# Performance work log

Hardware: AMD Instinct MI355X
Metric: run time of the kernel (lower is better)

## Reference

```python
import jax, jax.numpy as jnp
import numpy as np

K = 9
SIGMA = 4.0
RADIUS = 16  # round(4*sigma)
IMAGE_SHAPE = (256, 256)


def _gaussian_kernel_1d():
    i = jnp.arange(2 * RADIUS + 1, dtype=jnp.float32) - RADIUS
    g = jnp.exp(-(i ** 2) / (2.0 * SIGMA ** 2))
    return g / jnp.sum(g)


def _gaussian_blur(x):
    # x: [b, H, W, 1]; separable Gaussian blur, reflect-101 borders (cv2 default)
    g = _gaussian_kernel_1d()
    xp = jnp.pad(x, ((0, 0), (RADIUS, RADIUS), (RADIUS, RADIUS), (0, 0)), mode='reflect')
    dn = ('NHWC', 'HWIO', 'NHWC')
    kv = g.reshape(2 * RADIUS + 1, 1, 1, 1)  # vertical pass
    kh = g.reshape(1, 2 * RADIUS + 1, 1, 1)  # horizontal pass
    y = jax.lax.conv_general_dilated(xp, kv, (1, 1), 'VALID', dimension_numbers=dn)
    y = jax.lax.conv_general_dilated(y, kh, (1, 1), 'VALID', dimension_numbers=dn)
    return y


def setup_inputs() -> dict:
    key = jax.random.key(0)
    k1, k2 = jax.random.split(key)
    inputs = jax.random.normal(k1, (8, 32, 32, 512), dtype=jnp.float32)
    feature_vector = jax.random.normal(k2, (16384, 512), dtype=jnp.float32)
    return {"inputs": inputs, "feature_vector": feature_vector}


def reference(inputs, feature_vector):
    b, h, w, c = inputs.shape
    feat = inputs.reshape(b * h * w, c)
    # pairwise euclidean distances: [b*h*w, N]
    d2 = (jnp.sum(feat ** 2, axis=-1, keepdims=True)
          + jnp.sum(feature_vector ** 2, axis=-1)[None, :]
          - 2.0 * feat @ feature_vector.T)
    dist = jnp.sqrt(jnp.maximum(d2, 0.0))
    # k smallest distances, ascending (equivalent to tf.sort(...)[..., :k])
    neg_topk, _ = jax.lax.top_k(-dist, K)
    score = -neg_topk  # [b*h*w, K], ascending
    mask = score[:, 0].reshape(b, h, w, 1)
    score = score.reshape(b, h * w, K)
    # patch with maximal nearest-neighbor distance
    idx = jnp.argmax(score[..., 0], axis=-1)  # [b]
    conf = jnp.take_along_axis(score, idx[:, None, None], axis=1)[:, 0, :]  # [b, K]
    exp_conf = jnp.exp(conf)
    weight = 1.0 - jnp.max(exp_conf, axis=-1) / jnp.sum(exp_conf, axis=-1)
    score_out = (jnp.max(score[..., 0], axis=-1) * weight)[:, None]  # [b, 1]
    mask = jax.image.resize(mask, (b, *IMAGE_SHAPE, 1), method='bilinear', antialias=False)
    mask = _gaussian_blur(mask)
    return score_out, mask
```

## Files before the change

### kernel.cpp

```cpp
#include <hip/hip_runtime.h>

typedef __attribute__((ext_vector_type(8))) short bf16x8;
typedef __attribute__((ext_vector_type(4))) float f32x4;

static constexpr int M = 8192;
static constexpr int N = 16384;
static constexpr int K = 512;
static constexpr int BM = 128;
static constexpr int BN = 128;
static constexpr int BK = 32;
static constexpr int KSTEPS = K / BK;
static constexpr int RBLK = M / BM;
static constexpr int CBLK = N / BN;
static constexpr int BMs = 128;
static constexpr int BKs = 64;
static constexpr int KCHUNKS_S = K / BKs;
static constexpr int NGROUPS_S = 8;
static constexpr int GROUP_N_S = N / NGROUPS_S;
static constexpr int NTILES_S = GROUP_N_S / 128;
static constexpr float F_INF = 3.0e38f;

__device__ __forceinline__ unsigned short f2bf(float f) {
    unsigned int u = __float_as_uint(f);
    return (unsigned short)((u + 0x7fffu + ((u >> 16) & 1u)) >> 16);
}

__device__ __forceinline__ void gl_lds16(const unsigned short* g, unsigned short* l) {
    __builtin_amdgcn_global_load_lds(
        (const __attribute__((address_space(1))) unsigned int*)g,
        (__attribute__((address_space(3))) unsigned int*)l, 16, 0, 0);
}

__global__ void k_prep(const float* __restrict__ Q, const float* __restrict__ F,
                       unsigned short* __restrict__ Qb, unsigned short* __restrict__ Fb,
                       float* __restrict__ qn, float* __restrict__ fn) {
    int wid = blockIdx.x * 4 + (threadIdx.x >> 6);
    int lane = threadIdx.x & 63;
    bool isQ = wid < M;
    const float* src = isQ ? (Q + (size_t)wid * K) : (F + (size_t)(wid - M) * K);
    unsigned short* dst = isQ ? (Qb + (size_t)wid * K) : (Fb + (size_t)(wid - M) * K);
    const float4* p = reinterpret_cast<const float4*>(src) + lane * 2;
    float4 a = p[0], b = p[1];
    float s = a.x*a.x + a.y*a.y + a.z*a.z + a.w*a.w
            + b.x*b.x + b.y*b.y + b.z*b.z + b.w*b.w;
    bf16x8 v;
    v[0]=(short)f2bf(a.x); v[1]=(short)f2bf(a.y); v[2]=(short)f2bf(a.z); v[3]=(short)f2bf(a.w);
    v[4]=(short)f2bf(b.x); v[5]=(short)f2bf(b.y); v[6]=(short)f2bf(b.z); v[7]=(short)f2bf(b.w);
    *reinterpret_cast<bf16x8*>(dst + lane * 8) = v;
    #pragma unroll
    for (int d = 1; d < 64; d <<= 1) s += __shfl_xor(s, d);
    if (lane == 0) { if (isQ) qn[wid] = s; else fn[wid - M] = s; }
}

__global__ void k_norms(const float* __restrict__ Q, const float* __restrict__ F,
                        float* __restrict__ qn, float* __restrict__ fn) {
    int wid = blockIdx.x * 4 + (threadIdx.x >> 6);
    int lane = threadIdx.x & 63;
    const float* src = (wid < M) ? (Q + (size_t)wid * K) : (F + (size_t)(wid - M) * K);
    const float4* p = reinterpret_cast<const float4*>(src) + lane * 2;
    float4 a = p[0], b = p[1];
    float s = a.x*a.x + a.y*a.y + a.z*a.z + a.w*a.w
            + b.x*b.x + b.y*b.y + b.z*b.z + b.w*b.w;
    #pragma unroll
    for (int d = 1; d < 64; d <<= 1) s += __shfl_xor(s, d);
    if (lane == 0) { if (wid < M) qn[wid] = s; else fn[wid - M] = s; }
}

__global__ __launch_bounds__(256, 4)
void k_mingemm4(const unsigned short* __restrict__ Qb, const unsigned short* __restrict__ Fb,
                const float* __restrict__ qn, const float* __restrict__ fn,
                float* __restrict__ pv, unsigned int* __restrict__ pi) {
    __shared__ unsigned short As[2][BM * BK];
    __shared__ unsigned short Bs[2][BN * BK];
    __shared__ float redv[BM][2];
    __shared__ unsigned int redi[BM][2];

    const int tid = threadIdx.x;
    const int lane = tid & 63;
    const int wave = tid >> 6;
    const int wr = wave >> 1, wc = wave & 1;
    const int l15 = lane & 15, l4 = lane >> 4;

    const int wg = blockIdx.x;
    const int x = wg & 7, q = wg >> 3;
    const int c_blk = x * 16 + (q & 15);
    const int r_blk = q >> 4;
    const int row0 = r_blk * BM;
    const int col0 = c_blk * BN;

    const int row_l = lane >> 2, p4 = lane & 3;
    const int g4 = p4 ^ (row_l & 3);
    const unsigned short* gA[2];
    const unsigned short* gB[2];
    #pragma unroll
    for (int i = 0; i < 2; ++i) {
        int row = wave * 32 + i * 16 + row_l;
        gA[i] = Qb + (size_t)(row0 + row) * K + g4 * 8;
        gB[i] = Fb + (size_t)(col0 + row) * K + g4 * 8;
    }

    auto stage = [&](int kc, int buf) {
        #pragma unroll
        for (int i = 0; i < 2; ++i) gl_lds16(gA[i] + kc * BK, &As[buf][(wave*32 + i*16) * BK]);
        #pragma unroll
        for (int i = 0; i < 2; ++i) gl_lds16(gB[i] + kc * BK, &Bs[buf][(wave*32 + i*16) * BK]);
    };

    f32x4 acc[4][4];
    #pragma unroll
    for (int a = 0; a < 4; ++a)
        #pragma unroll
        for (int b = 0; b < 4; ++b) acc[a][b] = f32x4{0.f, 0.f, 0.f, 0.f};

    stage(0, 0);
    __syncthreads();

    int cur = 0;
    for (int kc = 0; kc < KSTEPS; ++kc) {
        if (kc + 1 < KSTEPS) stage(kc + 1, cur ^ 1);
        __builtin_amdgcn_sched_barrier(0);
        const int gidx = l4;
        bf16x8 af[4], bfv[4];
        #pragma unroll
        for (int fi = 0; fi < 4; ++fi) {
            int r = wr*64 + fi*16 + l15;
            int pg = gidx ^ (r & 3);
            af[fi] = *reinterpret_cast<const bf16x8*>(&As[cur][r*BK + pg*8]);
        }
        #pragma unroll
        for (int fj = 0; fj < 4; ++fj) {
            int r = wc*64 + fj*16 + l15;
            int pg = gidx ^ (r & 3);
            bfv[fj] = *reinterpret_cast<const bf16x8*>(&Bs[cur][r*BK + pg*8]);
        }
        __builtin_amdgcn_s_setprio(1);
        #pragma unroll
        for (int fi = 0; fi < 4; ++fi)
            #pragma unroll
            for (int fj = 0; fj < 4; ++fj)
                acc[fi][fj] = __builtin_amdgcn_mfma_f32_16x16x32_bf16(
                    af[fi], bfv[fj], acc[fi][fj], 0, 0, 0);
        __builtin_amdgcn_s_setprio(0);
        __syncthreads();
        cur ^= 1;
    }

    float fnv[4];
    #pragma unroll
    for (int fj = 0; fj < 4; ++fj) fnv[fj] = fn[col0 + wc*64 + fj*16 + l15];
    #pragma unroll
    for (int fi = 0; fi < 4; ++fi) {
        #pragma unroll
        for (int j = 0; j < 4; ++j) {
            int rloc = wr*64 + fi*16 + l4*4 + j;
            float qv = qn[row0 + rloc];
            float v = F_INF; unsigned int ix = 0;
            #pragma unroll
            for (int fj = 0; fj < 4; ++fj) {
                float d2 = qv + fnv[fj] - 2.0f * acc[fi][fj][j];
                if (d2 < v) { v = d2; ix = (unsigned int)(col0 + wc*64 + fj*16 + l15); }
            }
            #pragma unroll
            for (int d = 1; d < 16; d <<= 1) {
                float ov = __shfl_xor(v, d);
                unsigned int oi = (unsigned int)__shfl_xor((int)ix, d);
                if (ov < v) { v = ov; ix = oi; }
            }
            if (l15 == 0) { redv[rloc][wc] = v; redi[rloc][wc] = ix; }
        }
    }
    __syncthreads();
    if (tid < BM) {
        float v = redv[tid][0]; unsigned int ix = redi[tid][0];
        if (redv[tid][1] < v) { v = redv[tid][1]; ix = redi[tid][1]; }
        pv[(size_t)(row0 + tid) * CBLK + c_blk] = v;
        pi[(size_t)(row0 + tid) * CBLK + c_blk] = ix;
    }
}

__global__ __launch_bounds__(256, 2)
void k_mingemm_cast(const float* __restrict__ Q, const float* __restrict__ F,
                    const float* __restrict__ qn, const float* __restrict__ fn,
                    float* __restrict__ pv, unsigned int* __restrict__ pi) {
    __shared__ unsigned short As[BMs * BKs];
    __shared__ unsigned short Bs[BMs * BKs];
    __shared__ float qn_t[BMs];
    __shared__ float fn_t[BMs];

    const int tid = threadIdx.x;
    const int lane = tid & 63;
    const int wave = tid >> 6;
    const int wr = wave >> 1, wc = wave & 1;
    const int l15 = lane & 15, l4 = lane >> 4;

    const int row0 = blockIdx.x * BMs;
    const int gbase = blockIdx.y * GROUP_N_S;

    const int srow = tid >> 3;
    const int p8 = tid & 7;
    const int g8 = p8 ^ (srow & 7);
    const float* pA[4];
    const float* pB[4];
    int dstOff[4];
    #pragma unroll
    for (int i = 0; i < 4; ++i) {
        int r = i * 32 + srow;
        pA[i] = Q + (size_t)(row0 + r) * K + g8 * 8;
        pB[i] = F + (size_t)(gbase + r) * K + g8 * 8;
        dstOff[i] = r * BKs + p8 * 8;
    }

    float mval[4][4];
    unsigned int midx[4][4];
    float qnv[4][4];
    #pragma unroll
    for (int a = 0; a < 4; ++a)
        #pragma unroll
        for (int b = 0; b < 4; ++b) { mval[a][b] = F_INF; midx[a][b] = 0; qnv[a][b] = 0.f; }

    for (int nt = 0; nt < NTILES_S; ++nt) {
        f32x4 acc[4][4];
        #pragma unroll
        for (int a = 0; a < 4; ++a)
            #pragma unroll
            for (int b = 0; b < 4; ++b) acc[a][b] = f32x4{0.f, 0.f, 0.f, 0.f};

        for (int kc = 0; kc < KCHUNKS_S; ++kc) {
            __syncthreads();
            #pragma unroll
            for (int i = 0; i < 4; ++i) {
                const float4* sa = reinterpret_cast<const float4*>(pA[i] + kc * BKs);
                float4 xa = sa[0], ya = sa[1];
                const float4* sb = reinterpret_cast<const float4*>(pB[i] + nt * (128 * K) + kc * BKs);
                float4 xb = sb[0], yb = sb[1];
                bf16x8 va, vb;
                va[0]=(short)f2bf(xa.x); va[1]=(short)f2bf(xa.y); va[2]=(short)f2bf(xa.z); va[3]=(short)f2bf(xa.w);
                va[4]=(short)f2bf(ya.x); va[5]=(short)f2bf(ya.y); va[6]=(short)f2bf(ya.z); va[7]=(short)f2bf(ya.w);
                vb[0]=(short)f2bf(xb.x); vb[1]=(short)f2bf(xb.y); vb[2]=(short)f2bf(xb.z); vb[3]=(short)f2bf(xb.w);
                vb[4]=(short)f2bf(yb.x); vb[5]=(short)f2bf(yb.y); vb[6]=(short)f2bf(yb.z); vb[7]=(short)f2bf(yb.w);
                *reinterpret_cast<bf16x8*>(&As[dstOff[i]]) = va;
                *reinterpret_cast<bf16x8*>(&Bs[dstOff[i]]) = vb;
            }
            if (kc == 0) {
                if (nt == 0 && tid < BMs) qn_t[tid] = qn[row0 + tid];
                if (tid < 128) fn_t[tid] = fn[gbase + nt * 128 + tid];
            }
            __syncthreads();
            if (nt == 0 && kc == 0) {
                #pragma unroll
                for (int fi = 0; fi < 4; ++fi)
                    #pragma unroll
                    for (int j = 0; j < 4; ++j)
                        qnv[fi][j] = qn_t[wr*64 + fi*16 + l4*4 + j];
            }
            #pragma unroll
            for (int ks = 0; ks < 2; ++ks) {
                const int gidx = ks * 4 + l4;
                bf16x8 af[4], bfv[4];
                #pragma unroll
                for (int fi = 0; fi < 4; ++fi) {
                    int r = wr*64 + fi*16 + l15;
                    int pg = gidx ^ (r & 7);
                    af[fi] = *reinterpret_cast<const bf16x8*>(&As[r*BKs + pg*8]);
                }
                #pragma unroll
                for (int fj = 0; fj < 4; ++fj) {
                    int r = wc*64 + fj*16 + l15;
                    int pg = gidx ^ (r & 7);
                    bfv[fj] = *reinterpret_cast<const bf16x8*>(&Bs[r*BKs + pg*8]);
                }
                #pragma unroll
                for (int fi = 0; fi < 4; ++fi)
                    #pragma unroll
                    for (int fj = 0; fj < 4; ++fj)
                        acc[fi][fj] = __builtin_amdgcn_mfma_f32_16x16x32_bf16(
                            af[fi], bfv[fj], acc[fi][fj], 0, 0, 0);
            }
        }
        const int colb = gbase + nt * 128 + wc * 64;
        float fnv[4];
        #pragma unroll
        for (int fj = 0; fj < 4; ++fj) fnv[fj] = fn_t[wc*64 + fj*16 + l15];
        #pragma unroll
        for (int fi = 0; fi < 4; ++fi) {
            #pragma unroll
            for (int j = 0; j < 4; ++j) {
                float qv = qnv[fi][j];
                #pragma unroll
                for (int fj = 0; fj < 4; ++fj) {
                    float d2 = qv + fnv[fj] - 2.0f * acc[fi][fj][j];
                    if (d2 < mval[fi][j]) {
                        mval[fi][j] = d2;
                        midx[fi][j] = (unsigned int)(colb + fj*16 + l15);
                    }
                }
            }
        }
    }
    #pragma unroll
    for (int fi = 0; fi < 4; ++fi) {
        #pragma unroll
        for (int j = 0; j < 4; ++j) {
            float v = mval[fi][j];
            unsigned int ix = midx[fi][j];
            #pragma unroll
            for (int d = 1; d < 16; d <<= 1) {
                float ov = __shfl_xor(v, d);
                unsigned int oi = (unsigned int)__shfl_xor((int)ix, d);
                if (ov < v) { v = ov; ix = oi; }
            }
            if (l15 == 0) {
                int rg = row0 + wr*64 + fi*16 + l4*4 + j;
                int pidx = rg * 16 + blockIdx.y * 2 + wc;
                pv[pidx] = v;
                pi[pidx] = ix;
            }
        }
    }
}

__global__ void k_refine(const float* __restrict__ Q, const float* __restrict__ F,
                         const float* __restrict__ pv, const unsigned int* __restrict__ pi,
                         float* __restrict__ minD, int PS) {
    int row = blockIdx.x * 4 + (threadIdx.x >> 6);
    int lane = threadIdx.x & 63;
    float v = F_INF; unsigned int ix = 0;
    for (int t = lane; t < PS; t += 64) {
        float nv = pv[(size_t)row*PS + t];
        if (nv < v) { v = nv; ix = pi[(size_t)row*PS + t]; }
    }
    #pragma unroll
    for (int d = 1; d < 64; d <<= 1) {
        float ov = __shfl_xor(v, d);
        unsigned int oi = (unsigned int)__shfl_xor((int)ix, d);
        if (ov < v) { v = ov; ix = oi; }
    }
    const float4* q = reinterpret_cast<const float4*>(Q + (size_t)row * K) + lane*2;
    const float4* f = reinterpret_cast<const float4*>(F + (size_t)ix * K) + lane*2;
    float4 a0 = q[0], a1 = q[1], b0 = f[0], b1 = f[1];
    float s = 0.f, dx;
    dx = a0.x-b0.x; s += dx*dx;  dx = a0.y-b0.y; s += dx*dx;
    dx = a0.z-b0.z; s += dx*dx;  dx = a0.w-b0.w; s += dx*dx;
    dx = a1.x-b1.x; s += dx*dx;  dx = a1.y-b1.y; s += dx*dx;
    dx = a1.z-b1.z; s += dx*dx;  dx = a1.w-b1.w; s += dx*dx;
    #pragma unroll
    for (int d = 1; d < 64; d <<= 1) s += __shfl_xor(s, d);
    if (lane == 0) minD[row] = sqrtf(s);
}

__global__ void k_argmax(const float* __restrict__ minD, unsigned int* __restrict__ sel) {
    __shared__ float sv[256];
    __shared__ int si[256];
    int b = blockIdx.x, tid = threadIdx.x;
    float bv = -F_INF; int bi = 0;
    for (int p = tid; p < 1024; p += 256) {
        float v = minD[b*1024 + p];
        if (v > bv) { bv = v; bi = p; }
    }
    sv[tid] = bv; si[tid] = bi;
    __syncthreads();
    for (int s = 128; s > 0; s >>= 1) {
        if (tid < s) {
            if (sv[tid+s] > sv[tid] || (sv[tid+s] == sv[tid] && si[tid+s] < si[tid])) {
                sv[tid] = sv[tid+s]; si[tid] = si[tid+s];
            }
        }
        __syncthreads();
    }
    if (tid == 0) sel[b] = (unsigned int)(b*1024 + si[0]);
}

__global__ void k_dist8(const float* __restrict__ Q, const float* __restrict__ F,
                        const unsigned int* __restrict__ sel, float* __restrict__ d2all) {
    __shared__ float qs[8][512];
    int tid = threadIdx.x;
    int lane = tid & 63, wave = tid >> 6;
    for (int i = tid; i < 8*512; i += 256) {
        int b = i >> 9;
        qs[b][i & 511] = Q[(size_t)sel[b] * K + (i & 511)];
    }
    __syncthreads();
    int base = blockIdx.x * 128 + wave * 32;
    for (int r = 0; r < 32; ++r) {
        int row = base + r;
        const float4* fp = reinterpret_cast<const float4*>(F + (size_t)row * K) + lane*2;
        float4 f0 = fp[0], f1 = fp[1];
        float fv[8] = {f0.x,f0.y,f0.z,f0.w,f1.x,f1.y,f1.z,f1.w};
        float accb[8];
        #pragma unroll
        for (int b = 0; b < 8; ++b) {
            float s = 0.f;
            #pragma unroll
            for (int e = 0; e < 8; ++e) {
                float d = fv[e] - qs[b][lane*8 + e];
                s += d * d;
            }
            accb[b] = s;
        }
        #pragma unroll
        for (int d = 1; d < 64; d <<= 1)
            #pragma unroll
            for (int b = 0; b < 8; ++b) accb[b] += __shfl_xor(accb[b], d);
        if (lane == 0) {
            #pragma unroll
            for (int b = 0; b < 8; ++b) d2all[b * N + row] = accb[b];
        }
    }
}

__global__ void k_sel9(const float* __restrict__ d2all, float* __restrict__ out) {
    __shared__ float sv[256 * 10];
    int b = blockIdx.x, tid = threadIdx.x;
    float v[9];
    #pragma unroll
    for (int i = 0; i < 9; ++i) v[i] = F_INF;
    for (int i = tid; i < N; i += 256) {
        float x = d2all[b * N + i];
        #pragma unroll
        for (int s = 0; s < 9; ++s) {
            float lo = fminf(v[s], x), hi = fmaxf(v[s], x);
            v[s] = lo; x = hi;
        }
    }
    #pragma unroll
    for (int i = 0; i < 9; ++i) sv[tid*10 + i] = v[i];
    sv[tid*10 + 9] = F_INF;
    __syncthreads();
    for (int s = 128; s > 0; s >>= 1) {
        if (tid < s) {
            int ia = 1, ib = 1;
            float av = sv[tid*10], bv = sv[(tid+s)*10];
            float c[9];
            #pragma unroll
            for (int k = 0; k < 9; ++k) {
                bool ta = av <= bv;
                c[k] = ta ? av : bv;
                float na = sv[tid*10 + ia], nb = sv[(tid+s)*10 + ib];
                if (ta) { av = na; ++ia; } else { bv = nb; ++ib; }
            }
            #pragma unroll
            for (int k = 0; k < 9; ++k) sv[tid*10 + k] = c[k];
        }
        __syncthreads();
    }
    if (tid == 0) {
        float c[9];
        #pragma unroll
        for (int i = 0; i < 9; ++i) c[i] = sqrtf(fmaxf(sv[i], 0.f));
        float S = 0.f;
        #pragma unroll
        for (int i = 0; i < 9; ++i) S += expf(c[i] - c[8]);
        out[b] = c[0] * (1.f - 1.f / S);
    }
}

__global__ void k_top9(const float* __restrict__ Q, const float* __restrict__ F,
                       const unsigned int* __restrict__ sel, float* __restrict__ part9) {
    __shared__ float qs[512];
    __shared__ float dist[2048];
    __shared__ float rv[256];
    __shared__ int ri[256];
    int b = blockIdx.x >> 3, g = blockIdx.x & 7;
    int tid = threadIdx.x;
    unsigned int srow = sel[b];
    if (tid < 128)
        reinterpret_cast<float4*>(qs)[tid] =
            reinterpret_cast<const float4*>(Q + (size_t)srow * K)[tid];
    __syncthreads();
    #pragma unroll
    for (int e = 0; e < 8; ++e) {
        int fl = tid + 256*e;
        const float* fp = F + (size_t)(g*2048 + fl) * K;
        float s = 0.f;
        for (int k = 0; k < 512; k += 4) {
            float4 fv4 = *reinterpret_cast<const float4*>(fp + k);
            float d0 = qs[k]   - fv4.x;
            float d1 = qs[k+1] - fv4.y;
            float d2 = qs[k+2] - fv4.z;
            float d3 = qs[k+3] - fv4.w;
            s += d0*d0 + d1*d1 + d2*d2 + d3*d3;
        }
        dist[fl] = s;
    }
    __syncthreads();
    for (int it = 0; it < 9; ++it) {
        float lv = F_INF; int li = 0;
        #pragma unroll
        for (int e = 0; e < 8; ++e) {
            int idx = tid + 256*e;
            float v = dist[idx];
            if (v < lv) { lv = v; li = idx; }
        }
        rv[tid] = lv; ri[tid] = li;
        __syncthreads();
        for (int s = 128; s > 0; s >>= 1) {
            if (tid < s && rv[tid+s] < rv[tid]) { rv[tid] = rv[tid+s]; ri[tid] = ri[tid+s]; }
            __syncthreads();
        }
        if (tid == 0) {
            part9[(b*8+g)*9 + it] = rv[0];
            dist[ri[0]] = F_INF;
        }
        __syncthreads();
    }
}

__global__ void k_final(const float* __restrict__ part9, float* __restrict__ out) {
    int b = threadIdx.x;
    if (b >= 8) return;
    float arr[9];
    #pragma unroll
    for (int i = 0; i < 9; ++i) arr[i] = F_INF;
    for (int g = 0; g < 8; ++g)
        for (int i = 0; i < 9; ++i) {
            float v = part9[(b*8+g)*9 + i];
            #pragma unroll
            for (int s = 0; s < 9; ++s) {
                float lo = fminf(arr[s], v), hi = fmaxf(arr[s], v);
                arr[s] = lo; v = hi;
            }
        }
    float c[9];
    #pragma unroll
    for (int i = 0; i < 9; ++i) c[i] = sqrtf(fmaxf(arr[i], 0.f));
    float c8 = c[8], S = 0.f;
    #pragma unroll
    for (int i = 0; i < 9; ++i) S += expf(c[i] - c8);
    float w = 1.f - 1.f / S;
    out[b] = c[0] * w;
}

__global__ void k_wmat(float* __restrict__ W) {
    int idx = blockIdx.x * 256 + threadIdx.x;
    int o = idx >> 5, j = idx & 31;
    float gsum = 0.f;
    #pragma unroll
    for (int u = 0; u < 33; ++u) { float d = (float)(u - 16); gsum += expf(-d*d * (1.f/32.f)); }
    float acc = 0.f;
    for (int u = 0; u < 33; ++u) {
        float d = (float)(u - 16);
        float gu = expf(-d*d * (1.f/32.f));
        int y = o + u - 16;
        y = y < 0 ? -y : (y > 255 ? 510 - y : y);
        float xin = ((float)y + 0.5f) * 0.125f - 0.5f;
        float j0f = floorf(xin);
        int j0 = (int)j0f;
        float wfr = xin - j0f;
        float r;
        if (j0 < 0) r = (j == 0) ? 1.f : 0.f;
        else if (j0 >= 31) r = (j == 31) ? 1.f : 0.f;
        else r = (j == j0) ? (1.f - wfr) : ((j == j0 + 1) ? wfr : 0.f);
        acc += gu * r;
    }
    W[idx] = acc / gsum;
}

__global__ void k_mask(const float* __restrict__ minD, const float* __restrict__ W,
                       float* __restrict__ outm) {
    __shared__ float Ms[1024];
    __shared__ float Ws[8192];
    __shared__ float Ts[8192];
    int b = blockIdx.x, tid = threadIdx.x;
    for (int i = tid; i < 1024; i += 256) Ms[i] = minD[b*1024 + i];
    for (int i = tid; i < 8192; i += 256) Ws[i] = W[i];
    __syncthreads();
    {
        int o = tid;
        float wrow[32];
        #pragma unroll
        for (int i = 0; i < 32; ++i) wrow[i] = Ws[o*32 + i];
        for (int j = 0; j < 32; ++j) {
            float s = 0.f;
            #pragma unroll
            for (int i = 0; i < 32; ++i) s += wrow[i] * Ms[i*32 + j];
            Ts[o*32 + j] = s;
        }
    }
    __syncthreads();
    {
        int p = tid;
        float wp[32];
        #pragma unroll
        for (int j = 0; j < 32; ++j) wp[j] = Ws[p*32 + j];
        float* dst = outm + (size_t)b * 65536;
        for (int o = 0; o < 256; ++o) {
            float s = 0.f;
            #pragma unroll
            for (int j = 0; j < 32; ++j) s += Ts[o*32 + j] * wp[j];
            dst[o*256 + p] = s;
        }
    }
}

extern "C" void kernel_launch(void* const* d_in, const int* in_sizes, int n_in,
                              void* d_out, int out_size, void* d_ws, size_t ws_size,
                              hipStream_t stream) {
    const float* Q = (const float*)d_in[0];
    const float* F = (const float*)d_in[1];
    float* out = (float*)d_out;

    const size_t smallFloats = (size_t)8192*CBLK*2 + 8192 + 8 + 576 + (size_t)8*N + 8192 + 16384 + 8192;
    const size_t REQ = smallFloats*4 + (size_t)M*K*2 + (size_t)N*K*2;
    const bool fast = ws_size >= REQ;
    const int PS = fast ? CBLK : 16;

    float* ws = (float*)d_ws;
    float* pv = ws;
    unsigned int* pi = (unsigned int*)(pv + 8192*CBLK);
    float* minD = (float*)(pi + 8192*CBLK);
    unsigned int* sel = (unsigned int*)(minD + 8192);
    float* part9 = (float*)(sel + 8);
    float* d2all = part9 + 576;
    float* qn = d2all + (size_t)8*N;
    float* fn = qn + 8192;
    float* W  = fn + 16384;
    unsigned short* Qb = (unsigned short*)(W + 8192);
    unsigned short* Fb = Qb + (size_t)M*K;

    k_wmat <<<dim3(32), 256, 0, stream>>>(W);
    if (fast) {
        k_prep <<<dim3((M + N) / 4), 256, 0, stream>>>(Q, F, Qb, Fb, qn, fn);
        k_mingemm4<<<dim3(RBLK * CBLK), 256, 0, stream>>>(Qb, Fb, qn, fn, pv, pi);
        k_refine<<<dim3(M / 4), 256, 0, stream>>>(Q, F, pv, pi, minD, PS);
        k_argmax<<<dim3(8), 256, 0, stream>>>(minD, sel);
        k_dist8<<<dim3(N / 128), 256, 0, stream>>>(Q, F, sel, d2all);
        k_sel9 <<<dim3(8), 256, 0, stream>>>(d2all, out);
    } else {
        k_norms<<<dim3((M + N) / 4), 256, 0, stream>>>(Q, F, qn, fn);
        k_mingemm_cast<<<dim3(M / BMs, NGROUPS_S), 256, 0, stream>>>(Q, F, qn, fn, pv, pi);
        k_refine<<<dim3(M / 4), 256, 0, stream>>>(Q, F, pv, pi, minD, PS);
        k_argmax<<<dim3(8), 256, 0, stream>>>(minD, sel);
        k_top9 <<<dim3(64), 256, 0, stream>>>(Q, F, sel, part9);
        k_final<<<dim3(1), 64, 0, stream>>>(part9, out);
    }
    k_mask <<<dim3(8), 256, 0, stream>>>(minD, W, out + 8);
}
```

Baseline: 367.0 us.

## Enlarge min-GEMM tile to 256x256 and stream B fragments from global into registers

The distance GEMM moves to 256x256x64 tiles with 8 waves per block. B (the feature bank) is written by the prep kernel in a fragment-packed layout, so each wave loads its MFMA operands directly from global memory into registers with double buffering, skipping LDS. Only A is staged through LDS, using a wider XOR swizzle and manual vmcnt/barrier pipelining. This raises arithmetic intensity and cuts LDS traffic, at the cost of higher register pressure and a fragile hand-written wait-count schedule.

Measured after the change: 367.0 us. No clear change (-0.0%).

```diff
diff --git a/kernel.cpp b/kernel.cpp
--- a/kernel.cpp
+++ b/kernel.cpp
@@ -6,9 +6,9 @@
 static constexpr int M = 8192;
 static constexpr int N = 16384;
 static constexpr int K = 512;
-static constexpr int BM = 128;
-static constexpr int BN = 128;
-static constexpr int BK = 32;
+static constexpr int BM = 256;
+static constexpr int BN = 256;
+static constexpr int BK = 64;
 static constexpr int KSTEPS = K / BK;
 static constexpr int RBLK = M / BM;
 static constexpr int CBLK = N / BN;
@@ -31,14 +31,20 @@
         (__attribute__((address_space(3))) unsigned int*)l, 16, 0, 0);
 }
 
+__device__ __forceinline__ bf16x8 gload16(const unsigned short* base, unsigned int voff) {
+    bf16x8 r;
+    asm volatile("global_load_dwordx4 %0, %1, %2"
+                 : "=v"(r) : "v"(voff), "s"(base) : "memory");
+    return r;
+}
+
 __global__ void k_prep(const float* __restrict__ Q, const float* __restrict__ F,
-                       unsigned short* __restrict__ Qb, unsigned short* __restrict__ Fb,
+                       unsigned short* __restrict__ Qb, unsigned short* __restrict__ Fbf,
                        float* __restrict__ qn, float* __restrict__ fn) {
     int wid = blockIdx.x * 4 + (threadIdx.x >> 6);
     int lane = threadIdx.x & 63;
     bool isQ = wid < M;
     const float* src = isQ ? (Q + (size_t)wid * K) : (F + (size_t)(wid - M) * K);
-    unsigned short* dst = isQ ? (Qb + (size_t)wid * K) : (Fb + (size_t)(wid - M) * K);
     const float4* p = reinterpret_cast<const float4*>(src) + lane * 2;
     float4 a = p[0], b = p[1];
     float s = a.x*a.x + a.y*a.y + a.z*a.z + a.w*a.w
@@ -46,7 +52,13 @@
     bf16x8 v;
     v[0]=(short)f2bf(a.x); v[1]=(short)f2bf(a.y); v[2]=(short)f2bf(a.z); v[3]=(short)f2bf(a.w);
     v[4]=(short)f2bf(b.x); v[5]=(short)f2bf(b.y); v[6]=(short)f2bf(b.z); v[7]=(short)f2bf(b.w);
-    *reinterpret_cast<bf16x8*>(dst + lane * 8) = v;
+    if (isQ) {
+        *reinterpret_cast<bf16x8*>(Qb + (size_t)wid * K + lane * 8) = v;
+    } else {
+        int f = wid - M;
+        size_t off = ((size_t)(f >> 4) * 16 + (lane >> 2)) * 512 + (f & 15) * 32 + (lane & 3) * 8;
+        *reinterpret_cast<bf16x8*>(Fbf + off) = v;
+    }
     #pragma unroll
     for (int d = 1; d < 64; d <<= 1) s += __shfl_xor(s, d);
     if (lane == 0) { if (isQ) qn[wid] = s; else fn[wid - M] = s; }
@@ -66,93 +78,140 @@
     if (lane == 0) { if (wid < M) qn[wid] = s; else fn[wid - M] = s; }
 }
 
-__global__ __launch_bounds__(256, 4)
-void k_mingemm4(const unsigned short* __restrict__ Qb, const unsigned short* __restrict__ Fb,
+__global__ __launch_bounds__(512, 2)
+void k_mingemm5(const unsigned short* __restrict__ Qb, const unsigned short* __restrict__ Fbf,
                 const float* __restrict__ qn, const float* __restrict__ fn,
                 float* __restrict__ pv, unsigned int* __restrict__ pi) {
     __shared__ unsigned short As[2][BM * BK];
-    __shared__ unsigned short Bs[2][BN * BK];
-    __shared__ float redv[BM][2];
-    __shared__ unsigned int redi[BM][2];
+    __shared__ float redv[BM][4];
+    __shared__ unsigned int redi[BM][4];
 
     const int tid = threadIdx.x;
     const int lane = tid & 63;
     const int wave = tid >> 6;
-    const int wr = wave >> 1, wc = wave & 1;
+    const int wr = wave >> 2;
+    const int wc = wave & 3;
     const int l15 = lane & 15, l4 = lane >> 4;
 
     const int wg = blockIdx.x;
     const int x = wg & 7, q = wg >> 3;
-    const int c_blk = x * 16 + (q & 15);
-    const int r_blk = q >> 4;
+    const int c_blk = x * 8 + (q & 7);
+    const int r_blk = q >> 3;
     const int row0 = r_blk * BM;
     const int col0 = c_blk * BN;
 
-    const int row_l = lane >> 2, p4 = lane & 3;
-    const int g4 = p4 ^ (row_l & 3);
-    const unsigned short* gA[2];
-    const unsigned short* gB[2];
-    #pragma unroll
-    for (int i = 0; i < 2; ++i) {
-        int row = wave * 32 + i * 16 + row_l;
-        gA[i] = Qb + (size_t)(row0 + row) * K + g4 * 8;
-        gB[i] = Fb + (size_t)(col0 + row) * K + g4 * 8;
-    }
-
-    auto stage = [&](int kc, int buf) {
-        #pragma unroll
-        for (int i = 0; i < 2; ++i) gl_lds16(gA[i] + kc * BK, &As[buf][(wave*32 + i*16) * BK]);
-        #pragma unroll
-        for (int i = 0; i < 2; ++i) gl_lds16(gB[i] + kc * BK, &Bs[buf][(wave*32 + i*16) * BK]);
-    };
-
-    f32x4 acc[4][4];
-    #pragma unroll
-    for (int a = 0; a < 4; ++a)
+    const int r_l = lane >> 3, p8 = lane & 7;
+    const int g8 = p8 ^ r_l;
+    const unsigned short* gA[4];
+    #pragma unroll
+    for (int i = 0; i < 4; ++i) {
+        int row = wave * 32 + i * 8 + r_l;
+        gA[i] = Qb + (size_t)(row0 + row) * K + g8 * 8;
+    }
+
+    unsigned int voffB[4][2];
+    #pragma unroll
+    for (int fj = 0; fj < 4; ++fj) {
+        unsigned int nblk = (unsigned int)(c_blk * 16 + wc * 4 + fj);
+        #pragma unroll
+        for (int ks = 0; ks < 2; ++ks)
+            voffB[fj][ks] = (nblk * 16 + ks) * 1024 + l15 * 64 + l4 * 16;
+    }
+
+    f32x4 acc[8][4];
+    #pragma unroll
+    for (int a = 0; a < 8; ++a)
         #pragma unroll
         for (int b = 0; b < 4; ++b) acc[a][b] = f32x4{0.f, 0.f, 0.f, 0.f};
 
-    stage(0, 0);
-    __syncthreads();
-
-    int cur = 0;
-    for (int kc = 0; kc < KSTEPS; ++kc) {
-        if (kc + 1 < KSTEPS) stage(kc + 1, cur ^ 1);
-        __builtin_amdgcn_sched_barrier(0);
-        const int gidx = l4;
-        bf16x8 af[4], bfv[4];
-        #pragma unroll
-        for (int fi = 0; fi < 4; ++fi) {
-            int r = wr*64 + fi*16 + l15;
-            int pg = gidx ^ (r & 3);
-            af[fi] = *reinterpret_cast<const bf16x8*>(&As[cur][r*BK + pg*8]);
-        }
-        #pragma unroll
-        for (int fj = 0; fj < 4; ++fj) {
-            int r = wc*64 + fj*16 + l15;
-            int pg = gidx ^ (r & 3);
-            bfv[fj] = *reinterpret_cast<const bf16x8*>(&Bs[cur][r*BK + pg*8]);
-        }
-        __builtin_amdgcn_s_setprio(1);
-        #pragma unroll
-        for (int fi = 0; fi < 4; ++fi)
-            #pragma unroll
-            for (int fj = 0; fj < 4; ++fj)
-                acc[fi][fj] = __builtin_amdgcn_mfma_f32_16x16x32_bf16(
-                    af[fi], bfv[fj], acc[fi][fj], 0, 0, 0);
-        __builtin_amdgcn_s_setprio(0);
-        __syncthreads();
-        cur ^= 1;
-    }
-
+    bf16x8 b0[4][2], b1[4][2];
+
+    #pragma unroll
+    for (int fj = 0; fj < 4; ++fj) {
+        b0[fj][0] = gload16(Fbf, voffB[fj][0]);
+        b0[fj][1] = gload16(Fbf, voffB[fj][1]);
+    }
+    #pragma unroll
+    for (int i = 0; i < 4; ++i) gl_lds16(gA[i], &As[0][(wave*32 + i*8) * BK]);
+
+#define GSTEP(T, BCUR, BNXT, P) do {                                              \
+    if ((T) < KSTEPS - 1) {                                                       \
+        _Pragma("unroll")                                                         \
+        for (int fj = 0; fj < 4; ++fj) {                                          \
+            BNXT[fj][0] = gload16(Fbf, voffB[fj][0] + ((T)+1)*2048u);             \
+            BNXT[fj][1] = gload16(Fbf, voffB[fj][1] + ((T)+1)*2048u);             \
+        }                                                                         \
+        _Pragma("unroll")                                                         \
+        for (int i = 0; i < 4; ++i)                                               \
+            gl_lds16(gA[i] + ((T)+1)*BK, &As[1-(P)][(wave*32 + i*8) * BK]);       \
+        asm volatile("s_waitcnt vmcnt(12)" ::: "memory");                         \
+    } else {                                                                      \
+        asm volatile("s_waitcnt vmcnt(0)" ::: "memory");                          \
+    }                                                                             \
+    __builtin_amdgcn_sched_barrier(0);                                            \
+    __builtin_amdgcn_s_barrier();                   \
+    __builtin_amdgcn_sched_barrier(0);                                            \
+    {                                                                             \
+        bf16x8 af0[8];                                                            \
+        _Pragma("unroll")                                                         \
+        for (int fi = 0; fi < 8; ++fi) {                                          \
+            int r = wr*128 + fi*16 + l15;                                         \
+            int pg = l4 ^ (r & 7);                                                \
+            af0[fi] = *reinterpret_cast<const bf16x8*>(&As[P][r*BK + pg*8]);      \
+        }                                                                         \
+        asm volatile("s_waitcnt lgkmcnt(0)" ::: "memory");                        \
+        __builtin_amdgcn_sched_barrier(0);                                        \
+        __builtin_amdgcn_s_setprio(1);                                            \
+        _Pragma("unroll")                                                         \
+        for (int fi = 0; fi < 8; ++fi)                                            \
+            _Pragma("unroll")                                                     \
+            for (int fj = 0; fj < 4; ++fj)                                        \
+                acc[fi][fj] = __builtin_amdgcn_mfma_f32_16x16x32_bf16(            \
+                    af0[fi], BCUR[fj][0], acc[fi][fj], 0, 0, 0);                  \
+        __builtin_amdgcn_s_setprio(0);                                            \
+    }                                                                             \
+    {                                                                             \
+        bf16x8 af1[8];                                                            \
+        _Pragma("unroll")                                                         \
+        for (int fi = 0; fi < 8; ++fi) {                                          \
+            int r = wr*128 + fi*16 + l15;                                         \
+            int pg = (4 + l4) ^ (r & 7);                                          \
+            af1[fi] = *reinterpret_cast<const bf16x8*>(&As[P][r*BK + pg*8]);      \
+        }                                                                         \
+        asm volatile("s_waitcnt lgkmcnt(0)" ::: "memory");                        \
+        __builtin_amdgcn_sched_barrier(0);                                        \
+        __builtin_amdgcn_s_barrier();                \
+        __builtin_amdgcn_sched_barrier(0);                                        \
+        __builtin_amdgcn_s_setprio(1);                                            \
+        _Pragma("unroll")                                                         \
+        for (int fi = 0; fi < 8; ++fi)                                            \
+            _Pragma("unroll")                                                     \
+            for (int fj = 0; fj < 4; ++fj)                                        \
+                acc[fi][fj] = __builtin_amdgcn_mfma_f32_16x16x32_bf16(            \
+                    af1[fi], BCUR[fj][1], acc[fi][fj], 0, 0, 0);                  \
+        __builtin_amdgcn_s_setprio(0);                                            \
+    }                                                                             \
+} while (0)
+
+    GSTEP(0, b0, b1, 0);
+    GSTEP(1, b1, b0, 1);
+    GSTEP(2, b0, b1, 0);
+    GSTEP(3, b1, b0, 1);
+    GSTEP(4, b0, b1, 0);
+    GSTEP(5, b1, b0, 1);
+    GSTEP(6, b0, b1, 0);
+    GSTEP(7, b1, b0, 1);
+#undef GSTEP
+
+    __syncthreads();
     float fnv[4];
     #pragma unroll
     for (int fj = 0; fj < 4; ++fj) fnv[fj] = fn[col0 + wc*64 + fj*16 + l15];
     #pragma unroll
-    for (int fi = 0; fi < 4; ++fi) {
+    for (int fi = 0; fi < 8; ++fi) {
         #pragma unroll
         for (int j = 0; j < 4; ++j) {
-            int rloc = wr*64 + fi*16 + l4*4 + j;
+            int rloc = wr*128 + fi*16 + l4*4 + j;
             float qv = qn[row0 + rloc];
             float v = F_INF; unsigned int ix = 0;
             #pragma unroll
@@ -172,7 +231,11 @@
     __syncthreads();
     if (tid < BM) {
         float v = redv[tid][0]; unsigned int ix = redi[tid][0];
-        if (redv[tid][1] < v) { v = redv[tid][1]; ix = redi[tid][1]; }
+        #pragma unroll
+        for (int w2 = 1; w2 < 4; ++w2) {
+            float ov = redv[tid][w2];
+            if (ov < v) { v = ov; ix = redi[tid][w2]; }
+        }
         pv[(size_t)(row0 + tid) * CBLK + c_blk] = v;
         pi[(size_t)(row0 + tid) * CBLK + c_blk] = ix;
     }
@@ -615,12 +678,12 @@
     float* fn = qn + 8192;
     float* W  = fn + 16384;
     unsigned short* Qb = (unsigned short*)(W + 8192);
-    unsigned short* Fb = Qb + (size_t)M*K;
+    unsigned short* Fbf = Qb + (size_t)M*K;
 
     k_wmat <<<dim3(32), 256, 0, stream>>>(W);
     if (fast) {
-        k_prep <<<dim3((M + N) / 4), 256, 0, stream>>>(Q, F, Qb, Fb, qn, fn);
-        k_mingemm4<<<dim3(RBLK * CBLK), 256, 0, stream>>>(Qb, Fb, qn, fn, pv, pi);
+        k_prep <<<dim3((M + N) / 4), 256, 0, stream>>>(Q, F, Qb, Fbf, qn, fn);
+        k_mingemm5<<<dim3(RBLK * CBLK), 512, 0, stream>>>(Qb, Fbf, qn, fn, pv, pi);
         k_refine<<<dim3(M / 4), 256, 0, stream>>>(Q, F, pv, pi, minD, PS);
         k_argmax<<<dim3(8), 256, 0, stream>>>(minD, sel);
         k_dist8<<<dim3(N / 128), 256, 0, stream>>>(Q, F, sel, d2all);
```

## Replace 128x128 min-GEMM with 256x256 8-wave ping-pong pipelined kernel

Applied to the files above, without the earlier changes.

Replaces the 4-wave 128x128-tile bf16 min-distance GEMM with an 8-wave 256x256-tile kernel. It uses BK=64 chunks split into half-tiles and streams them into LDS through a multi-stage global_load_lds schedule. Explicit s_barrier/vmcnt phases interleave MFMA work with prefetch. The larger tiles raise arithmetic intensity and halve the number of per-row partial minima that k_refine must scan, at the cost of more registers, more LDS, one block per CU, and a fragile hand-scheduled pipeline.

Measured after the change: 355.8 us. 3.0% less time.

```diff
diff --git a/kernel.cpp b/kernel.cpp
--- a/kernel.cpp
+++ b/kernel.cpp
@@ -6,10 +6,8 @@
 static constexpr int M = 8192;
 static constexpr int N = 16384;
 static constexpr int K = 512;
-static constexpr int BM = 128;
-static constexpr int BN = 128;
-static constexpr int BK = 32;
-static constexpr int KSTEPS = K / BK;
+static constexpr int BM = 256;
+static constexpr int BN = 256;
 static constexpr int RBLK = M / BM;
 static constexpr int CBLK = N / BN;
 static constexpr int BMs = 128;
@@ -25,7 +23,7 @@
     return (unsigned short)((u + 0x7fffu + ((u >> 16) & 1u)) >> 16);
 }
 
-__device__ __forceinline__ void gl_lds16(const unsigned short* g, unsigned short* l) {
+__device__ __forceinline__ void gl_lds16(const void* g, void* l) {
     __builtin_amdgcn_global_load_lds(
         (const __attribute__((address_space(1))) unsigned int*)g,
         (__attribute__((address_space(3))) unsigned int*)l, 16, 0, 0);
@@ -66,99 +64,152 @@
     if (lane == 0) { if (wid < M) qn[wid] = s; else fn[wid - M] = s; }
 }
 
-__global__ __launch_bounds__(256, 4)
-void k_mingemm4(const unsigned short* __restrict__ Qb, const unsigned short* __restrict__ Fb,
+__global__ __launch_bounds__(512, 1)
+void k_mingemm8(const unsigned short* __restrict__ Qb, const unsigned short* __restrict__ Fb,
                 const float* __restrict__ qn, const float* __restrict__ fn,
                 float* __restrict__ pv, unsigned int* __restrict__ pi) {
-    __shared__ unsigned short As[2][BM * BK];
-    __shared__ unsigned short Bs[2][BN * BK];
-    __shared__ float redv[BM][2];
-    __shared__ unsigned int redi[BM][2];
+    __shared__ unsigned short As[2][2][8192];
+    __shared__ unsigned short Bs[2][2][8192];
+    __shared__ float redv[256][4];
+    __shared__ unsigned int redi[256][4];
 
     const int tid = threadIdx.x;
     const int lane = tid & 63;
     const int wave = tid >> 6;
-    const int wr = wave >> 1, wc = wave & 1;
-    const int l15 = lane & 15, l4 = lane >> 4;
+    const int wr = wave >> 2;
+    const int wc = wave & 3;
+    const int l15 = lane & 15, l4 = lane >> 4, l7 = lane & 7;
+    const int r3 = lane >> 3;
+    const int g8 = (lane & 7) ^ (r3 & 7);
 
     const int wg = blockIdx.x;
     const int x = wg & 7, q = wg >> 3;
-    const int c_blk = x * 16 + (q & 15);
-    const int r_blk = q >> 4;
+    const int c_blk = x * 8 + (q & 7);
+    const int r_blk = q >> 3;
     const int row0 = r_blk * BM;
     const int col0 = c_blk * BN;
 
-    const int row_l = lane >> 2, p4 = lane & 3;
-    const int g4 = p4 ^ (row_l & 3);
-    const unsigned short* gA[2];
-    const unsigned short* gB[2];
-    #pragma unroll
-    for (int i = 0; i < 2; ++i) {
-        int row = wave * 32 + i * 16 + row_l;
-        gA[i] = Qb + (size_t)(row0 + row) * K + g4 * 8;
-        gB[i] = Fb + (size_t)(col0 + row) * K + g4 * 8;
-    }
-
-    auto stage = [&](int kc, int buf) {
-        #pragma unroll
-        for (int i = 0; i < 2; ++i) gl_lds16(gA[i] + kc * BK, &As[buf][(wave*32 + i*16) * BK]);
-        #pragma unroll
-        for (int i = 0; i < 2; ++i) gl_lds16(gB[i] + kc * BK, &Bs[buf][(wave*32 + i*16) * BK]);
-    };
-
-    f32x4 acc[4][4];
-    #pragma unroll
-    for (int a = 0; a < 4; ++a)
+#define STAGE_A(t, hh) do {                                                        \
+    _Pragma("unroll")                                                              \
+    for (int i = 0; i < 2; ++i)                                                    \
+        gl_lds16(Qb + (size_t)(row0 + (hh)*128 + i*64 + wave*8 + r3) * K           \
+                    + (t)*64 + g8*8,                                               \
+                 &As[(t)&1][hh][(i*64 + wave*8) * 64]);                            \
+} while (0)
+#define STAGE_B(t, hh) do {                                                        \
+    _Pragma("unroll")                                                              \
+    for (int i = 0; i < 2; ++i)                                                    \
+        gl_lds16(Fb + (size_t)(col0 + (hh)*128 + i*64 + wave*8 + r3) * K           \
+                    + (t)*64 + g8*8,                                               \
+                 &Bs[(t)&1][hh][(i*64 + wave*8) * 64]);                            \
+} while (0)
+
+    f32x4 acc[8][4];
+    #pragma unroll
+    for (int a = 0; a < 8; ++a)
         #pragma unroll
         for (int b = 0; b < 4; ++b) acc[a][b] = f32x4{0.f, 0.f, 0.f, 0.f};
 
-    stage(0, 0);
-    __syncthreads();
-
-    int cur = 0;
-    for (int kc = 0; kc < KSTEPS; ++kc) {
-        if (kc + 1 < KSTEPS) stage(kc + 1, cur ^ 1);
-        __builtin_amdgcn_sched_barrier(0);
-        const int gidx = l4;
-        bf16x8 af[4], bfv[4];
-        #pragma unroll
-        for (int fi = 0; fi < 4; ++fi) {
-            int r = wr*64 + fi*16 + l15;
-            int pg = gidx ^ (r & 3);
-            af[fi] = *reinterpret_cast<const bf16x8*>(&As[cur][r*BK + pg*8]);
-        }
-        #pragma unroll
-        for (int fj = 0; fj < 4; ++fj) {
-            int r = wc*64 + fj*16 + l15;
-            int pg = gidx ^ (r & 3);
-            bfv[fj] = *reinterpret_cast<const bf16x8*>(&Bs[cur][r*BK + pg*8]);
-        }
-        __builtin_amdgcn_s_setprio(1);
-        #pragma unroll
-        for (int fi = 0; fi < 4; ++fi)
-            #pragma unroll
-            for (int fj = 0; fj < 4; ++fj)
-                acc[fi][fj] = __builtin_amdgcn_mfma_f32_16x16x32_bf16(
-                    af[fi], bfv[fj], acc[fi][fj], 0, 0, 0);
-        __builtin_amdgcn_s_setprio(0);
-        __syncthreads();
-        cur ^= 1;
-    }
+    bf16x8 afr[4][2], bfr[4][2];
+
+#define PHASE(t, s, STMT, VMN) do {                                                \
+    STMT;                                                                          \
+    if ((s) == 0) {                                                                \
+        _Pragma("unroll")                                                          \
+        for (int f = 0; f < 4; ++f)                                                \
+            _Pragma("unroll")                                                      \
+            for (int ks = 0; ks < 2; ++ks)                                         \
+                afr[f][ks] = *reinterpret_cast<const bf16x8*>(                     \
+                    &As[(t)&1][wr][(f*16 + l15)*64 + (((ks*4 + l4) ^ l7))*8]);     \
+        _Pragma("unroll")                                                          \
+        for (int f = 0; f < 4; ++f)                                                \
+            _Pragma("unroll")                                                      \
+            for (int ks = 0; ks < 2; ++ks)                                         \
+                bfr[f][ks] = *reinterpret_cast<const bf16x8*>(                     \
+                    &Bs[(t)&1][f >> 1][(wc*32 + (f & 1)*16 + l15)*64               \
+                                       + (((ks*4 + l4) ^ l7))*8]);                 \
+    } else if ((s) == 2) {                                                         \
+        _Pragma("unroll")                                                          \
+        for (int f = 0; f < 4; ++f)                                                \
+            _Pragma("unroll")                                                      \
+            for (int ks = 0; ks < 2; ++ks)                                         \
+                afr[f][ks] = *reinterpret_cast<const bf16x8*>(                     \
+                    &As[(t)&1][wr][((f+4)*16 + l15)*64 + (((ks*4 + l4) ^ l7))*8]); \
+    }                                                                              \
+    __builtin_amdgcn_s_barrier();                                                  \
+    if ((s) == 0 || (s) == 2) {                                                    \
+        asm volatile("s_waitcnt lgkmcnt(0)" ::: "memory");                         \
+        __builtin_amdgcn_sched_barrier(0);                                         \
+    }                                                                              \
+    __builtin_amdgcn_s_setprio(1);                                                 \
+    {                                                                              \
+        const int AB = ((s) >= 2) ? 4 : 0;                                         \
+        const int FJ = ((s) & 1) ? 2 : 0;                                          \
+        _Pragma("unroll")                                                          \
+        for (int f = 0; f < 4; ++f)                                                \
+            _Pragma("unroll")                                                      \
+            for (int j2 = 0; j2 < 2; ++j2)                                         \
+                _Pragma("unroll")                                                  \
+                for (int ks = 0; ks < 2; ++ks)                                     \
+                    acc[AB + f][FJ + j2] = __builtin_amdgcn_mfma_f32_16x16x32_bf16(\
+                        afr[f][ks], bfr[FJ + j2][ks], acc[AB + f][FJ + j2], 0,0,0);\
+    }                                                                              \
+    __builtin_amdgcn_s_setprio(0);                                                 \
+    asm volatile("s_waitcnt vmcnt(" #VMN ")" ::: "memory");                        \
+    __builtin_amdgcn_sched_barrier(0);                                             \
+    __builtin_amdgcn_s_barrier();                                                  \
+} while (0)
+
+    STAGE_B(0, 0); STAGE_B(0, 1); STAGE_A(0, 0); STAGE_A(0, 1);
+    STAGE_B(1, 0); STAGE_B(1, 1); STAGE_A(1, 0);
+    asm volatile("s_waitcnt vmcnt(6)" ::: "memory");
+    __builtin_amdgcn_sched_barrier(0);
+    __builtin_amdgcn_s_barrier();
+
+#define ITER(T)                                        \
+    PHASE(T,     0, STAGE_A((T)+1, 1), 6);             \
+    PHASE(T,     1, STAGE_B((T)+2, 0), 6);             \
+    PHASE(T,     2, STAGE_B((T)+2, 1), 6);             \
+    PHASE(T,     3, STAGE_A((T)+2, 0), 6);             \
+    PHASE((T)+1, 0, STAGE_A((T)+2, 1), 6);             \
+    PHASE((T)+1, 1, STAGE_B((T)+3, 0), 6);             \
+    PHASE((T)+1, 2, STAGE_B((T)+3, 1), 6);             \
+    PHASE((T)+1, 3, STAGE_A((T)+3, 0), 6);
+
+    ITER(0)
+    ITER(2)
+    ITER(4)
+    PHASE(6, 0, STAGE_A(7, 1), 6);
+    PHASE(6, 1, (void)0, 6);
+    PHASE(6, 2, (void)0, 6);
+    PHASE(6, 3, (void)0, 0);
+    PHASE(7, 0, (void)0, 0);
+    PHASE(7, 1, (void)0, 0);
+    PHASE(7, 2, (void)0, 0);
+    PHASE(7, 3, (void)0, 0);
+#undef ITER
+#undef PHASE
+#undef STAGE_A
+#undef STAGE_B
 
     float fnv[4];
-    #pragma unroll
-    for (int fj = 0; fj < 4; ++fj) fnv[fj] = fn[col0 + wc*64 + fj*16 + l15];
-    #pragma unroll
-    for (int fi = 0; fi < 4; ++fi) {
+    int colg[4];
+    #pragma unroll
+    for (int fj = 0; fj < 4; ++fj) {
+        colg[fj] = col0 + (fj < 2 ? wc*32 + fj*16 : 128 + wc*32 + (fj - 2)*16) + l15;
+        fnv[fj] = fn[colg[fj]];
+    }
+    #pragma unroll
+    for (int fi = 0; fi < 8; ++fi) {
         #pragma unroll
         for (int j = 0; j < 4; ++j) {
-            int rloc = wr*64 + fi*16 + l4*4 + j;
+            int rloc = wr*128 + fi*16 + l4*4 + j;
             float qv = qn[row0 + rloc];
             float v = F_INF; unsigned int ix = 0;
             #pragma unroll
             for (int fj = 0; fj < 4; ++fj) {
                 float d2 = qv + fnv[fj] - 2.0f * acc[fi][fj][j];
-                if (d2 < v) { v = d2; ix = (unsigned int)(col0 + wc*64 + fj*16 + l15); }
+                if (d2 < v) { v = d2; ix = (unsigned int)colg[fj]; }
             }
             #pragma unroll
             for (int d = 1; d < 16; d <<= 1) {
@@ -172,7 +223,11 @@
     __syncthreads();
     if (tid < BM) {
         float v = redv[tid][0]; unsigned int ix = redi[tid][0];
-        if (redv[tid][1] < v) { v = redv[tid][1]; ix = redi[tid][1]; }
+        #pragma unroll
+        for (int w2 = 1; w2 < 4; ++w2) {
+            float ov = redv[tid][w2];
+            if (ov < v) { v = ov; ix = redi[tid][w2]; }
+        }
         pv[(size_t)(row0 + tid) * CBLK + c_blk] = v;
         pi[(size_t)(row0 + tid) * CBLK + c_blk] = ix;
     }
@@ -599,15 +654,14 @@
     const float* F = (const float*)d_in[1];
     float* out = (float*)d_out;
 
-    const size_t smallFloats = (size_t)8192*CBLK*2 + 8192 + 8 + 576 + (size_t)8*N + 8192 + 16384 + 8192;
+    const size_t smallFloats = (size_t)8192*64*2 + 8192 + 8 + 576 + (size_t)8*N + 8192 + 16384 + 8192;
     const size_t REQ = smallFloats*4 + (size_t)M*K*2 + (size_t)N*K*2;
     const bool fast = ws_size >= REQ;
-    const int PS = fast ? CBLK : 16;
 
     float* ws = (float*)d_ws;
     float* pv = ws;
-    unsigned int* pi = (unsigned int*)(pv + 8192*CBLK);
-    float* minD = (float*)(pi + 8192*CBLK);
+    unsigned int* pi = (unsigned int*)(pv + 8192*64);
+    float* minD = (float*)(pi + 8192*64);
     unsigned int* sel = (unsigned int*)(minD + 8192);
     float* part9 = (float*)(sel + 8);
     float* d2all = part9 + 576;
@@ -620,15 +674,15 @@
     k_wmat <<<dim3(32), 256, 0, stream>>>(W);
     if (fast) {
         k_prep <<<dim3((M + N) / 4), 256, 0, stream>>>(Q, F, Qb, Fb, qn, fn);
-        k_mingemm4<<<dim3(RBLK * CBLK), 256, 0, stream>>>(Qb, Fb, qn, fn, pv, pi);
-        k_refine<<<dim3(M / 4), 256, 0, stream>>>(Q, F, pv, pi, minD, PS);
+        k_mingemm8<<<dim3(RBLK * CBLK), 512, 0, stream>>>(Qb, Fb, qn, fn, pv, pi);
+        k_refine<<<dim3(M / 4), 256, 0, stream>>>(Q, F, pv, pi, minD, 64);
         k_argmax<<<dim3(8), 256, 0, stream>>>(minD, sel);
         k_dist8<<<dim3(N / 128), 256, 0, stream>>>(Q, F, sel, d2all);
         k_sel9 <<<dim3(8), 256, 0, stream>>>(d2all, out);
     } else {
         k_norms<<<dim3((M + N) / 4), 256, 0, stream>>>(Q, F, qn, fn);
         k_mingemm_cast<<<dim3(M / BMs, NGROUPS_S), 256, 0, stream>>>(Q, F, qn, fn, pv, pi);
-        k_refine<<<dim3(M / 4), 256, 0, stream>>>(Q, F, pv, pi, minD, PS);
+        k_refine<<<dim3(M / 4), 256, 0, stream>>>(Q, F, pv, pi, minD, 16);
         k_argmax<<<dim3(8), 256, 0, stream>>>(minD, sel);
         k_top9 <<<dim3(64), 256, 0, stream>>>(Q, F, sel, part9);
         k_final<<<dim3(1), 64, 0, stream>>>(part9, out);
```
